# Kernel optimization log

Measured on AMD Instinct MI355X. Metric: run time of the kernel, lower is better.

The kernel has to match this reference:

```python
import jax, jax.numpy as jnp
import numpy as np

N = 100000   # nodes
E = 1000000  # edges
D = 64       # feature dim (all layers)
K = 3        # hops


def setup_inputs() -> dict:
    key = jax.random.key(0)
    ks = jax.random.split(key, 8)
    y = jax.random.normal(ks[0], (N, D), dtype=jnp.float32)
    edge_index = jax.random.randint(ks[1], (2, E), 0, N, dtype=jnp.int64)
    edge_weight = jax.random.uniform(ks[2], (E,), dtype=jnp.float32)
    # TAGConv layer l has K+1 linear maps (no bias) plus one output bias.
    s = 1.0 / np.sqrt(D)
    W1 = jax.random.uniform(ks[3], (K + 1, D, D), dtype=jnp.float32, minval=-s, maxval=s)
    b1 = jax.random.uniform(ks[4], (D,), dtype=jnp.float32, minval=-s, maxval=s)
    W2 = jax.random.uniform(ks[5], (K + 1, D, D), dtype=jnp.float32, minval=-s, maxval=s)
    b2 = jax.random.uniform(ks[6], (D,), dtype=jnp.float32, minval=-s, maxval=s)
    return {"y": y, "edge_index": edge_index, "edge_weight": edge_weight,
            "W1": W1, "b1": b1, "W2": W2, "b2": b2}


def _tagconv(x, src, dst, ew, W, b):
    # out = sum_{k=0..K} (A^k x) W_k + b, where (A x)[i] = sum_{e: dst=i} ew_e * x[src_e]
    out = x @ W[0]
    h = x
    for k in range(1, K + 1):
        h = jax.ops.segment_sum(ew[:, None] * h[src], dst, num_segments=N)
        out = out + h @ W[k]
    return out + b


def reference(y, edge_index, edge_weight, W1, b1, W2, b2):
    src, dst = edge_index[0], edge_index[1]
    # layer 1: TAGConv -> residual (Identity) -> leaky_relu (primal=True path)
    h = _tagconv(y, src, dst, edge_weight, W1, b1)
    y = jax.nn.leaky_relu(h + y)
    # layer 2
    h = _tagconv(y, src, dst, edge_weight, W2, b2)
    y = jax.nn.leaky_relu(h + y)
    return y
```

## Files before the change

### kernel.cpp

```cpp
#include <hip/hip_runtime.h>
#include <cstdint>
#include <cstddef>

#define DFEAT 64
#define LSLOPE 0.01f
#define BINSHIFT 9
#define BINCAP 6144
#define CHUNK 4096

typedef _Float16 h8 __attribute__((ext_vector_type(8)));
typedef _Float16 h4 __attribute__((ext_vector_type(4)));
typedef _Float16 h2 __attribute__((ext_vector_type(2)));
typedef float f4 __attribute__((ext_vector_type(4)));

__global__ void setup_kernel(const unsigned int* __restrict__ ei, int* flag,
                             int* __restrict__ binCnt) {
  __shared__ int cnt;
  if (threadIdx.x == 0) cnt = 0;
  binCnt[threadIdx.x] = 0;
  __syncthreads();
  int z = 0;
  for (int i = threadIdx.x; i < 1024; i += blockDim.x)
    z += (ei[2 * i + 1] == 0u) ? 1 : 0;
  atomicAdd(&cnt, z);
  __syncthreads();
  if (threadIdx.x == 0) *flag = (cnt == 1024) ? 1 : 0;
}

__global__ void cvtprep_kernel(const float* __restrict__ in, _Float16* __restrict__ out,
                               int n4, const float* __restrict__ W1,
                               const float* __restrict__ W2, _Float16* __restrict__ Wt) {
  int i = blockIdx.x * blockDim.x + threadIdx.x;
  if (i < n4) {
    float4 v = ((const float4*)in)[i];
    h4 o;
    o[0] = (_Float16)v.x; o[1] = (_Float16)v.y;
    o[2] = (_Float16)v.z; o[3] = (_Float16)v.w;
    ((h4*)out)[i] = o;
  } else {
    int t = i - n4;
    if (t < 2 * 64 * 264) {
      int layer = t / (64 * 264);
      int r = t % (64 * 264);
      int c = r / 264;
      int kg = r % 264;
      float v = 0.f;
      if (kg < 256) {
        const float* W = layer ? W2 : W1;
        int a = kg >> 6, k = kg & 63;
        v = W[a * 4096 + k * 64 + c];
      }
      Wt[t] = (_Float16)v;
    }
  }
}

__global__ __launch_bounds__(256) void binA_kernel(
    const void* __restrict__ ei, const float* __restrict__ ew, int E,
    const int* __restrict__ flag, int* __restrict__ binCnt,
    int2* __restrict__ bins, int nbins) {
  __shared__ int hist[256];
  __shared__ int pref[256];
  __shared__ int lofs[256];
  __shared__ int gbase[256];
  __shared__ int2 pairs[CHUNK];
  int tid = threadIdx.x;
  int base = blockIdx.x * CHUNK;
  int nedge = E - base; if (nedge > CHUNK) nedge = CHUNK;
  for (int i = tid; i < nbins; i += 256) hist[i] = 0;
  __syncthreads();
  const bool is64 = (*flag != 0);
  for (int j = tid; j < nedge; j += 256) {
    int e = base + j;
    int d = is64 ? (int)((const long long*)ei)[(size_t)E + e]
                 : ((const int*)ei)[(size_t)E + e];
    atomicAdd(&hist[d >> BINSHIFT], 1);
  }
  __syncthreads();
  if (tid == 0) {
    int run = 0;
    for (int b = 0; b < nbins; ++b) { pref[b] = run; lofs[b] = run; run += hist[b]; }
  }
  __syncthreads();
  for (int j = tid; j < nedge; j += 256) {
    int e = base + j;
    int s, d;
    if (is64) { const long long* p = (const long long*)ei; s = (int)p[e]; d = (int)p[(size_t)E + e]; }
    else      { const int* p = (const int*)ei; s = p[e]; d = p[(size_t)E + e]; }
    int wq = (int)(ew[e] * 32768.0f + 0.5f);
    wq = wq > 32767 ? 32767 : wq;
    unsigned P = ((unsigned)s << 15) | (unsigned)wq;
    int pos = atomicAdd(&lofs[d >> BINSHIFT], 1);
    pairs[pos] = make_int2((int)P, d);
  }
  __syncthreads();
  for (int b = tid; b < nbins; b += 256)
    gbase[b] = (hist[b] > 0) ? atomicAdd(&binCnt[b], hist[b]) : 0;
  __syncthreads();
  for (int i = tid; i < nedge; i += 256) {
    int2 pr = pairs[i];
    int b = pr.y >> BINSHIFT;
    int off = gbase[b] + (i - pref[b]);
    if (off < BINCAP) bins[(size_t)b * BINCAP + off] = pr;
  }
}

__global__ __launch_bounds__(256) void binB_kernel(
    const int2* __restrict__ bins, const int* __restrict__ binCnt,
    int* __restrict__ rowptr, unsigned* __restrict__ ep, int nbins, int N) {
  __shared__ int ssum[256];
  __shared__ int cnt[512];
  __shared__ int ofs[512];
  int b = blockIdx.x, tid = threadIdx.x;
  ssum[tid] = (tid < nbins) ? binCnt[tid] : 0;
  __syncthreads();
  for (int off = 1; off < 256; off <<= 1) {
    int val = ssum[tid];
    int add = (tid >= off) ? ssum[tid - off] : 0;
    __syncthreads();
    ssum[tid] = val + add;
    __syncthreads();
  }
  int gstart = (b == 0) ? 0 : ssum[b - 1];
  if (b == nbins - 1 && tid == 0) rowptr[N] = ssum[nbins - 1];
  int nb = binCnt[b]; if (nb > BINCAP) nb = BINCAP;
  int dstBase = b << BINSHIFT;
  const int2* mybin = bins + (size_t)b * BINCAP;
  for (int i = tid; i < 512; i += 256) cnt[i] = 0;
  __syncthreads();
  for (int i = tid; i < nb; i += 256)
    atomicAdd(&cnt[mybin[i].y & 511], 1);
  __syncthreads();
  if (tid == 0) {
    int run = gstart;
    for (int k = 0; k < 512; ++k) { ofs[k] = run; run += cnt[k]; }
  }
  __syncthreads();
  for (int k = tid; k < 512; k += 256) {
    int d = dstBase + k;
    if (d < N) rowptr[d] = ofs[k];
  }
  __syncthreads();
  for (int i = tid; i < nb; i += 256) {
    int2 pr = mybin[i];
    int pos = atomicAdd(&ofs[pr.y & 511], 1);
    ep[pos] = (unsigned)pr.x;
  }
}

__device__ __forceinline__ void edge_fma(unsigned p, const uint4& v, float qs,
                                         h2& acc0, h2& acc1, h2& acc2, h2& acc3) {
  _Float16 wh = (_Float16)((float)(p & 32767u) * qs);
  h2 wp = {wh, wh};
  union { uint32_t u; h2 h; } cx, cy, cz, cw;
  cx.u = v.x; cy.u = v.y; cz.u = v.z; cw.u = v.w;
  acc0 += wp * cx.h; acc1 += wp * cy.h;
  acc2 += wp * cz.h; acc3 += wp * cw.h;
}

__global__ __launch_bounds__(256) void spmm_kernel(
    const _Float16* __restrict__ x, const int* __restrict__ rowptr,
    const unsigned* __restrict__ ep, _Float16* __restrict__ hout, int N) {
  int node = blockIdx.x * 32 + (threadIdx.x >> 3);
  if (node >= N) return;
  int fo = threadIdx.x & 7;
  int beg = rowptr[node], end = rowptr[node + 1];
  const float qs = 1.0f / 32768.0f;
  const uint4* __restrict__ xu = (const uint4*)x;
  h2 acc0 = {0, 0}, acc1 = {0, 0}, acc2 = {0, 0}, acc3 = {0, 0};
  int n = end - beg;
  if (n >= 4) {
    unsigned pa = ep[beg], pb = ep[beg + 1], pc = ep[beg + 2], pd = ep[beg + 3];
    uint4 va = xu[(size_t)(pa >> 15) * 8 + fo];
    uint4 vb = xu[(size_t)(pb >> 15) * 8 + fo];
    uint4 vc = xu[(size_t)(pc >> 15) * 8 + fo];
    uint4 vd = xu[(size_t)(pd >> 15) * 8 + fo];
    int i = beg + 4;
    for (; i + 3 < end; i += 4) {
      edge_fma(pa, va, qs, acc0, acc1, acc2, acc3);
      pa = ep[i];     va = xu[(size_t)(pa >> 15) * 8 + fo];
      edge_fma(pb, vb, qs, acc0, acc1, acc2, acc3);
      pb = ep[i + 1]; vb = xu[(size_t)(pb >> 15) * 8 + fo];
      edge_fma(pc, vc, qs, acc0, acc1, acc2, acc3);
      pc = ep[i + 2]; vc = xu[(size_t)(pc >> 15) * 8 + fo];
      edge_fma(pd, vd, qs, acc0, acc1, acc2, acc3);
      pd = ep[i + 3]; vd = xu[(size_t)(pd >> 15) * 8 + fo];
    }
    edge_fma(pa, va, qs, acc0, acc1, acc2, acc3);
    edge_fma(pb, vb, qs, acc0, acc1, acc2, acc3);
    edge_fma(pc, vc, qs, acc0, acc1, acc2, acc3);
    edge_fma(pd, vd, qs, acc0, acc1, acc2, acc3);
    for (; i < end; ++i) {
      unsigned p = ep[i];
      uint4 v = xu[(size_t)(p >> 15) * 8 + fo];
      edge_fma(p, v, qs, acc0, acc1, acc2, acc3);
    }
  } else {
    for (int i = beg; i < end; ++i) {
      unsigned p = ep[i];
      uint4 v = xu[(size_t)(p >> 15) * 8 + fo];
      edge_fma(p, v, qs, acc0, acc1, acc2, acc3);
    }
  }
  union { uint4 u; h2 h[4]; } o;
  o.h[0] = acc0; o.h[1] = acc1; o.h[2] = acc2; o.h[3] = acc3;
  ((uint4*)hout)[(size_t)node * 8 + fo] = o.u;
}

template <int OUTF16>
__global__ __launch_bounds__(256) void combine_mfma_kernel(
    const _Float16* __restrict__ x0, const _Float16* __restrict__ h1,
    const _Float16* __restrict__ h2v, const _Float16* __restrict__ h3,
    const _Float16* __restrict__ Wt, const float* __restrict__ b,
    const _Float16* __restrict__ resid, void* __restrict__ outp, int N) {
  __shared__ __align__(16) _Float16 Wl[64 * 264];

  int tid = threadIdx.x;
  {
    const uint32_t* g = (const uint32_t*)Wt;
    uint32_t* l = (uint32_t*)Wl;
    for (int i = tid; i < 64 * 132; i += 256) l[i] = g[i];
  }
  __syncthreads();

  int w = tid >> 6, lane = tid & 63;
  int l16 = lane & 15, lq = lane >> 4;
  int r0 = blockIdx.x * 128 + w * 32;

  f4 acc[2][4];
  f4 zero = {0.f, 0.f, 0.f, 0.f};
  #pragma unroll
  for (int rt = 0; rt < 2; ++rt)
    #pragma unroll
    for (int ct = 0; ct < 4; ++ct) acc[rt][ct] = zero;

  const _Float16* hops[4] = {x0, h1, h2v, h3};

  #pragma unroll
  for (int s = 0; s < 8; ++s) {
    const _Float16* __restrict__ Xa = hops[s >> 1];
    int kk = ((s & 1) << 5) + (lq << 3);
    int ra = r0 + l16;
    int rb = ra + 16;
    ra = ra < N ? ra : N - 1;
    rb = rb < N ? rb : N - 1;
    h8 A0 = *(const h8*)(Xa + (size_t)ra * DFEAT + kk);
    h8 A1 = *(const h8*)(Xa + (size_t)rb * DFEAT + kk);
    #pragma unroll
    for (int ct = 0; ct < 4; ++ct) {
      h8 B = *(const h8*)(Wl + (l16 + 16 * ct) * 264 + (s << 5) + (lq << 3));
      acc[0][ct] = __builtin_amdgcn_mfma_f32_16x16x32_f16(A0, B, acc[0][ct], 0, 0, 0);
      acc[1][ct] = __builtin_amdgcn_mfma_f32_16x16x32_f16(A1, B, acc[1][ct], 0, 0, 0);
    }
  }

  #pragma unroll
  for (int rt = 0; rt < 2; ++rt) {
    #pragma unroll
    for (int ct = 0; ct < 4; ++ct) {
      int col = 16 * ct + l16;
      float bb = b[col];
      #pragma unroll
      for (int reg = 0; reg < 4; ++reg) {
        int row = r0 + rt * 16 + lq * 4 + reg;
        if (row < N) {
          float v = acc[rt][ct][reg] + bb + (float)resid[(size_t)row * DFEAT + col];
          v = v > 0.f ? v : LSLOPE * v;
          if (OUTF16) ((_Float16*)outp)[(size_t)row * DFEAT + col] = (_Float16)v;
          else        ((float*)outp)[(size_t)row * DFEAT + col] = v;
        }
      }
    }
  }
}

extern "C" void kernel_launch(void* const* d_in, const int* in_sizes, int n_in,
                              void* d_out, int out_size, void* d_ws, size_t ws_size,
                              hipStream_t stream) {
  const float* y  = (const float*)d_in[0];
  const void*  ei = d_in[1];
  const float* ew = (const float*)d_in[2];
  const float* W1 = (const float*)d_in[3];
  const float* b1 = (const float*)d_in[4];
  const float* W2 = (const float*)d_in[5];
  const float* b2 = (const float*)d_in[6];
  float* out = (float*)d_out;

  const int N = in_sizes[0] / DFEAT;
  const int E = in_sizes[2];
  const size_t ND = (size_t)N * DFEAT;
  const int nbins = (N + (1 << BINSHIFT) - 1) >> BINSHIFT;

  _Float16* xh = (_Float16*)d_ws;
  _Float16* h1 = xh + ND;
  _Float16* h2b = h1 + ND;
  _Float16* h3 = h2b + ND;
  _Float16* o1 = h3 + ND;
  _Float16* Wt = o1 + ND;
  int* rowptr   = (int*)(((uintptr_t)(Wt + 2 * 64 * 264) + 255) & ~(uintptr_t)255);
  int* binCnt   = rowptr + (N + 1);
  int* flag     = binCnt + 256;
  int2* bins    = (int2*)(((uintptr_t)(flag + 1) + 255) & ~(uintptr_t)255);
  unsigned* ep  = (unsigned*)(bins + (size_t)nbins * BINCAP);

  const int n4 = (int)(ND / 4);
  const int cp_total = n4 + 2 * 64 * 264;

  setup_kernel<<<1, 256, 0, stream>>>((const unsigned int*)ei, flag, binCnt);
  cvtprep_kernel<<<(cp_total + 255) / 256, 256, 0, stream>>>(y, xh, n4, W1, W2, Wt);
  binA_kernel<<<(E + CHUNK - 1) / CHUNK, 256, 0, stream>>>(ei, ew, E, flag, binCnt, bins, nbins);
  binB_kernel<<<nbins, 256, 0, stream>>>(bins, binCnt, rowptr, ep, nbins, N);

  const int spmm_grid = (N + 31) / 32;
  const int comb_grid = (N + 127) / 128;

  spmm_kernel<<<spmm_grid, 256, 0, stream>>>(xh, rowptr, ep, h1, N);
  spmm_kernel<<<spmm_grid, 256, 0, stream>>>(h1, rowptr, ep, h2b, N);
  spmm_kernel<<<spmm_grid, 256, 0, stream>>>(h2b, rowptr, ep, h3, N);
  combine_mfma_kernel<1><<<comb_grid, 256, 0, stream>>>(xh, h1, h2b, h3, Wt, b1, xh, o1, N);
  spmm_kernel<<<spmm_grid, 256, 0, stream>>>(o1, rowptr, ep, h1, N);
  spmm_kernel<<<spmm_grid, 256, 0, stream>>>(h1, rowptr, ep, h2b, N);
  spmm_kernel<<<spmm_grid, 256, 0, stream>>>(h2b, rowptr, ep, h3, N);
  combine_mfma_kernel<0><<<comb_grid, 256, 0, stream>>>(o1, h1, h2b, h3, Wt + 64 * 264, b2, o1, out, N);
}
```

Measured before the change: 227.4 us.

## Fuse third-hop SpMM into the MFMA combine kernel via shared memory

The third SpMM hop is now computed inside the combine kernel. Each block gathers its 128 rows of the hop-3 result into an LDS tile, then runs the MFMA projection over all four hops, reading the first three from global memory. This removes one kernel launch per layer and the write and re-read of the h3 buffer. In exchange the combine kernel uses 512 threads with more LDS, and each wave now covers 16 rows instead of 32, so the SpMM gather and the MFMA work are serialized within a block.

```diff
diff --git a/kernel.cpp b/kernel.cpp
--- a/kernel.cpp
+++ b/kernel.cpp
@@ -158,15 +158,10 @@
   acc2 += wp * cz.h; acc3 += wp * cw.h;
 }
 
-__global__ __launch_bounds__(256) void spmm_kernel(
-    const _Float16* __restrict__ x, const int* __restrict__ rowptr,
-    const unsigned* __restrict__ ep, _Float16* __restrict__ hout, int N) {
-  int node = blockIdx.x * 32 + (threadIdx.x >> 3);
-  if (node >= N) return;
-  int fo = threadIdx.x & 7;
-  int beg = rowptr[node], end = rowptr[node + 1];
+__device__ __forceinline__ uint4 spmm_node(const uint4* __restrict__ xu,
+                                           const unsigned* __restrict__ ep,
+                                           int beg, int end, int fo) {
   const float qs = 1.0f / 32768.0f;
-  const uint4* __restrict__ xu = (const uint4*)x;
   h2 acc0 = {0, 0}, acc1 = {0, 0}, acc2 = {0, 0}, acc3 = {0, 0};
   int n = end - beg;
   if (n >= 4) {
@@ -204,71 +199,94 @@
   }
   union { uint4 u; h2 h[4]; } o;
   o.h[0] = acc0; o.h[1] = acc1; o.h[2] = acc2; o.h[3] = acc3;
-  ((uint4*)hout)[(size_t)node * 8 + fo] = o.u;
+  return o.u;
+}
+
+__global__ __launch_bounds__(256) void spmm_kernel(
+    const _Float16* __restrict__ x, const int* __restrict__ rowptr,
+    const unsigned* __restrict__ ep, _Float16* __restrict__ hout, int N) {
+  int node = blockIdx.x * 32 + (threadIdx.x >> 3);
+  if (node >= N) return;
+  int fo = threadIdx.x & 7;
+  uint4 r = spmm_node((const uint4*)x, ep, rowptr[node], rowptr[node + 1], fo);
+  ((uint4*)hout)[(size_t)node * 8 + fo] = r;
 }
 
 template <int OUTF16>
-__global__ __launch_bounds__(256) void combine_mfma_kernel(
+__global__ __launch_bounds__(512) void spmm_combine_kernel(
+    const _Float16* __restrict__ xg,
     const _Float16* __restrict__ x0, const _Float16* __restrict__ h1,
-    const _Float16* __restrict__ h2v, const _Float16* __restrict__ h3,
+    const _Float16* __restrict__ h2v,
+    const int* __restrict__ rowptr, const unsigned* __restrict__ ep,
     const _Float16* __restrict__ Wt, const float* __restrict__ b,
     const _Float16* __restrict__ resid, void* __restrict__ outp, int N) {
   __shared__ __align__(16) _Float16 Wl[64 * 264];
+  __shared__ __align__(16) _Float16 H3[128 * 72];
 
   int tid = threadIdx.x;
   {
     const uint32_t* g = (const uint32_t*)Wt;
     uint32_t* l = (uint32_t*)Wl;
-    for (int i = tid; i < 64 * 132; i += 256) l[i] = g[i];
+    for (int i = tid; i < 64 * 132; i += 512) l[i] = g[i];
+  }
+  {
+    int gid = tid >> 3, fo = tid & 7;
+    long long nb0 = (long long)blockIdx.x * 128;
+    #pragma unroll
+    for (int rep = 0; rep < 2; ++rep) {
+      int lr = gid + rep * 64;
+      long long node = nb0 + lr;
+      uint4 r = {0, 0, 0, 0};
+      if (node < N)
+        r = spmm_node((const uint4*)xg, ep, rowptr[node], rowptr[node + 1], fo);
+      *(uint4*)(H3 + lr * 72 + fo * 8) = r;
+    }
   }
   __syncthreads();
 
   int w = tid >> 6, lane = tid & 63;
   int l16 = lane & 15, lq = lane >> 4;
-  int r0 = blockIdx.x * 128 + w * 32;
-
-  f4 acc[2][4];
+  long long r0 = (long long)blockIdx.x * 128 + w * 16;
+  int lr0 = w * 16;
+
+  f4 acc[4];
   f4 zero = {0.f, 0.f, 0.f, 0.f};
   #pragma unroll
-  for (int rt = 0; rt < 2; ++rt)
-    #pragma unroll
-    for (int ct = 0; ct < 4; ++ct) acc[rt][ct] = zero;
-
-  const _Float16* hops[4] = {x0, h1, h2v, h3};
+  for (int ct = 0; ct < 4; ++ct) acc[ct] = zero;
+
+  const _Float16* hops[3] = {x0, h1, h2v};
 
   #pragma unroll
   for (int s = 0; s < 8; ++s) {
-    const _Float16* __restrict__ Xa = hops[s >> 1];
     int kk = ((s & 1) << 5) + (lq << 3);
-    int ra = r0 + l16;
-    int rb = ra + 16;
-    ra = ra < N ? ra : N - 1;
-    rb = rb < N ? rb : N - 1;
-    h8 A0 = *(const h8*)(Xa + (size_t)ra * DFEAT + kk);
-    h8 A1 = *(const h8*)(Xa + (size_t)rb * DFEAT + kk);
+    h8 A;
+    if (s < 6) {
+      const _Float16* __restrict__ Xa = hops[s >> 1];
+      long long ra = r0 + l16;
+      ra = ra < N ? ra : N - 1;
+      A = *(const h8*)(Xa + ra * DFEAT + kk);
+    } else {
+      A = *(const h8*)(H3 + (lr0 + l16) * 72 + kk);
+    }
     #pragma unroll
     for (int ct = 0; ct < 4; ++ct) {
       h8 B = *(const h8*)(Wl + (l16 + 16 * ct) * 264 + (s << 5) + (lq << 3));
-      acc[0][ct] = __builtin_amdgcn_mfma_f32_16x16x32_f16(A0, B, acc[0][ct], 0, 0, 0);
-      acc[1][ct] = __builtin_amdgcn_mfma_f32_16x16x32_f16(A1, B, acc[1][ct], 0, 0, 0);
+      acc[ct] = __builtin_amdgcn_mfma_f32_16x16x32_f16(A, B, acc[ct], 0, 0, 0);
     }
   }
 
   #pragma unroll
-  for (int rt = 0; rt < 2; ++rt) {
+  for (int ct = 0; ct < 4; ++ct) {
+    int col = 16 * ct + l16;
+    float bb = b[col];
     #pragma unroll
-    for (int ct = 0; ct < 4; ++ct) {
-      int col = 16 * ct + l16;
-      float bb = b[col];
-      #pragma unroll
-      for (int reg = 0; reg < 4; ++reg) {
-        int row = r0 + rt * 16 + lq * 4 + reg;
-        if (row < N) {
-          float v = acc[rt][ct][reg] + bb + (float)resid[(size_t)row * DFEAT + col];
-          v = v > 0.f ? v : LSLOPE * v;
-          if (OUTF16) ((_Float16*)outp)[(size_t)row * DFEAT + col] = (_Float16)v;
-          else        ((float*)outp)[(size_t)row * DFEAT + col] = v;
-        }
+    for (int reg = 0; reg < 4; ++reg) {
+      long long row = r0 + lq * 4 + reg;
+      if (row < N) {
+        float v = acc[ct][reg] + bb + (float)resid[row * DFEAT + col];
+        v = v > 0.f ? v : LSLOPE * v;
+        if (OUTF16) ((_Float16*)outp)[row * DFEAT + col] = (_Float16)v;
+        else        ((float*)outp)[row * DFEAT + col] = v;
       }
     }
   }
@@ -294,8 +312,7 @@
   _Float16* xh = (_Float16*)d_ws;
   _Float16* h1 = xh + ND;
   _Float16* h2b = h1 + ND;
-  _Float16* h3 = h2b + ND;
-  _Float16* o1 = h3 + ND;
+  _Float16* o1 = h2b + ND;
   _Float16* Wt = o1 + ND;
   int* rowptr   = (int*)(((uintptr_t)(Wt + 2 * 64 * 264) + 255) & ~(uintptr_t)255);
   int* binCnt   = rowptr + (N + 1);
@@ -316,10 +333,10 @@
 
   spmm_kernel<<<spmm_grid, 256, 0, stream>>>(xh, rowptr, ep, h1, N);
   spmm_kernel<<<spmm_grid, 256, 0, stream>>>(h1, rowptr, ep, h2b, N);
-  spmm_kernel<<<spmm_grid, 256, 0, stream>>>(h2b, rowptr, ep, h3, N);
-  combine_mfma_kernel<1><<<comb_grid, 256, 0, stream>>>(xh, h1, h2b, h3, Wt, b1, xh, o1, N);
+  spmm_combine_kernel<1><<<comb_grid, 512, 0, stream>>>(
+      h2b, xh, h1, h2b, rowptr, ep, Wt, b1, xh, o1, N);
   spmm_kernel<<<spmm_grid, 256, 0, stream>>>(o1, rowptr, ep, h1, N);
   spmm_kernel<<<spmm_grid, 256, 0, stream>>>(h1, rowptr, ep, h2b, N);
-  spmm_kernel<<<spmm_grid, 256, 0, stream>>>(h2b, rowptr, ep, h3, N);
-  combine_mfma_kernel<0><<<comb_grid, 256, 0, stream>>>(o1, h1, h2b, h3, Wt + 64 * 264, b2, o1, out, N);
-}
+  spmm_combine_kernel<0><<<comb_grid, 512, 0, stream>>>(
+      h2b, o1, h1, h2b, rowptr, ep, Wt + 64 * 264, b2, o1, out, N);
+}
```

Result: slower. 232.8 us (+2.3%).

## Fuse SpMM and combine stages into one cooperative persistent kernel

Applied to the files above, without the earlier changes.

Replaces the eight separate SpMM/combine kernel launches with a single cooperative mega-kernel that runs every stage as a grid-stride phase, separated by grid-wide syncs. The goal is to remove per-launch overhead and the idle tail between dependent kernels. The cost is a grid capped at 1024 blocks, a combine phase that reloads the weights into LDS on each call, 36KB of LDS held even during the SpMM phases, and grid.sync barrier overhead. Fewer resident blocks may also reduce the latency hiding available to the gather-bound SpMM.

```diff
diff --git a/kernel.cpp b/kernel.cpp
--- a/kernel.cpp
+++ b/kernel.cpp
@@ -1,6 +1,9 @@
 #include <hip/hip_runtime.h>
+#include <hip/hip_cooperative_groups.h>
 #include <cstdint>
 #include <cstddef>
+
+namespace cg = cooperative_groups;
 
 #define DFEAT 64
 #define LSLOPE 0.01f
@@ -158,15 +161,10 @@
   acc2 += wp * cz.h; acc3 += wp * cw.h;
 }
 
-__global__ __launch_bounds__(256) void spmm_kernel(
-    const _Float16* __restrict__ x, const int* __restrict__ rowptr,
-    const unsigned* __restrict__ ep, _Float16* __restrict__ hout, int N) {
-  int node = blockIdx.x * 32 + (threadIdx.x >> 3);
-  if (node >= N) return;
-  int fo = threadIdx.x & 7;
-  int beg = rowptr[node], end = rowptr[node + 1];
+__device__ __forceinline__ uint4 spmm_node(const uint4* __restrict__ xu,
+                                           const unsigned* __restrict__ ep,
+                                           int beg, int end, int fo) {
   const float qs = 1.0f / 32768.0f;
-  const uint4* __restrict__ xu = (const uint4*)x;
   h2 acc0 = {0, 0}, acc1 = {0, 0}, acc2 = {0, 0}, acc3 = {0, 0};
   int n = end - beg;
   if (n >= 4) {
@@ -204,17 +202,32 @@
   }
   union { uint4 u; h2 h[4]; } o;
   o.h[0] = acc0; o.h[1] = acc1; o.h[2] = acc2; o.h[3] = acc3;
-  ((uint4*)hout)[(size_t)node * 8 + fo] = o.u;
+  return o.u;
+}
+
+__device__ __forceinline__ void spmm_phase(const _Float16* __restrict__ x,
+                                           const int* __restrict__ rowptr,
+                                           const unsigned* __restrict__ ep,
+                                           _Float16* __restrict__ hout, int N) {
+  int fo = threadIdx.x & 7;
+  int lid = threadIdx.x >> 3;
+  for (long long base = (long long)blockIdx.x * 32; base < N;
+       base += (long long)gridDim.x * 32) {
+    long long node = base + lid;
+    if (node < N) {
+      uint4 r = spmm_node((const uint4*)x, ep, rowptr[node], rowptr[node + 1], fo);
+      ((uint4*)hout)[node * 8 + fo] = r;
+    }
+  }
 }
 
 template <int OUTF16>
-__global__ __launch_bounds__(256) void combine_mfma_kernel(
+__device__ __forceinline__ void combine_phase(
+    _Float16* __restrict__ Wl,
     const _Float16* __restrict__ x0, const _Float16* __restrict__ h1,
     const _Float16* __restrict__ h2v, const _Float16* __restrict__ h3,
     const _Float16* __restrict__ Wt, const float* __restrict__ b,
     const _Float16* __restrict__ resid, void* __restrict__ outp, int N) {
-  __shared__ __align__(16) _Float16 Wl[64 * 264];
-
   int tid = threadIdx.x;
   {
     const uint32_t* g = (const uint32_t*)Wt;
@@ -225,53 +238,80 @@
 
   int w = tid >> 6, lane = tid & 63;
   int l16 = lane & 15, lq = lane >> 4;
-  int r0 = blockIdx.x * 128 + w * 32;
-
-  f4 acc[2][4];
-  f4 zero = {0.f, 0.f, 0.f, 0.f};
-  #pragma unroll
-  for (int rt = 0; rt < 2; ++rt)
+  const _Float16* hops[4] = {x0, h1, h2v, h3};
+
+  for (long long t0 = (long long)blockIdx.x * 128; t0 < N;
+       t0 += (long long)gridDim.x * 128) {
+    long long r0 = t0 + w * 32;
+
+    f4 acc[2][4];
+    f4 zero = {0.f, 0.f, 0.f, 0.f};
     #pragma unroll
-    for (int ct = 0; ct < 4; ++ct) acc[rt][ct] = zero;
-
-  const _Float16* hops[4] = {x0, h1, h2v, h3};
-
-  #pragma unroll
-  for (int s = 0; s < 8; ++s) {
-    const _Float16* __restrict__ Xa = hops[s >> 1];
-    int kk = ((s & 1) << 5) + (lq << 3);
-    int ra = r0 + l16;
-    int rb = ra + 16;
-    ra = ra < N ? ra : N - 1;
-    rb = rb < N ? rb : N - 1;
-    h8 A0 = *(const h8*)(Xa + (size_t)ra * DFEAT + kk);
-    h8 A1 = *(const h8*)(Xa + (size_t)rb * DFEAT + kk);
+    for (int rt = 0; rt < 2; ++rt)
+      #pragma unroll
+      for (int ct = 0; ct < 4; ++ct) acc[rt][ct] = zero;
+
     #pragma unroll
-    for (int ct = 0; ct < 4; ++ct) {
-      h8 B = *(const h8*)(Wl + (l16 + 16 * ct) * 264 + (s << 5) + (lq << 3));
-      acc[0][ct] = __builtin_amdgcn_mfma_f32_16x16x32_f16(A0, B, acc[0][ct], 0, 0, 0);
-      acc[1][ct] = __builtin_amdgcn_mfma_f32_16x16x32_f16(A1, B, acc[1][ct], 0, 0, 0);
-    }
-  }
-
-  #pragma unroll
-  for (int rt = 0; rt < 2; ++rt) {
+    for (int s = 0; s < 8; ++s) {
+      const _Float16* __restrict__ Xa = hops[s >> 1];
+      int kk = ((s & 1) << 5) + (lq << 3);
+      long long ra = r0 + l16;
+      long long rb = ra + 16;
+      ra = ra < N ? ra : N - 1;
+      rb = rb < N ? rb : N - 1;
+      h8 A0 = *(const h8*)(Xa + ra * DFEAT + kk);
+      h8 A1 = *(const h8*)(Xa + rb * DFEAT + kk);
+      #pragma unroll
+      for (int ct = 0; ct < 4; ++ct) {
+        h8 B = *(const h8*)(Wl + (l16 + 16 * ct) * 264 + (s << 5) + (lq << 3));
+        acc[0][ct] = __builtin_amdgcn_mfma_f32_16x16x32_f16(A0, B, acc[0][ct], 0, 0, 0);
+        acc[1][ct] = __builtin_amdgcn_mfma_f32_16x16x32_f16(A1, B, acc[1][ct], 0, 0, 0);
+      }
+    }
+
     #pragma unroll
-    for (int ct = 0; ct < 4; ++ct) {
-      int col = 16 * ct + l16;
-      float bb = b[col];
+    for (int rt = 0; rt < 2; ++rt) {
       #pragma unroll
-      for (int reg = 0; reg < 4; ++reg) {
-        int row = r0 + rt * 16 + lq * 4 + reg;
-        if (row < N) {
-          float v = acc[rt][ct][reg] + bb + (float)resid[(size_t)row * DFEAT + col];
-          v = v > 0.f ? v : LSLOPE * v;
-          if (OUTF16) ((_Float16*)outp)[(size_t)row * DFEAT + col] = (_Float16)v;
-          else        ((float*)outp)[(size_t)row * DFEAT + col] = v;
+      for (int ct = 0; ct < 4; ++ct) {
+        int col = 16 * ct + l16;
+        float bb = b[col];
+        #pragma unroll
+        for (int reg = 0; reg < 4; ++reg) {
+          long long row = r0 + rt * 16 + lq * 4 + reg;
+          if (row < N) {
+            float v = acc[rt][ct][reg] + bb + (float)resid[row * DFEAT + col];
+            v = v > 0.f ? v : LSLOPE * v;
+            if (OUTF16) ((_Float16*)outp)[row * DFEAT + col] = (_Float16)v;
+            else        ((float*)outp)[row * DFEAT + col] = v;
+          }
         }
       }
     }
   }
+}
+
+__global__ void __launch_bounds__(256, 4) mega_kernel(
+    const _Float16* xh, _Float16* h1, _Float16* h2b, _Float16* h3, _Float16* o1,
+    float* out, const _Float16* Wt, const float* b1, const float* b2,
+    const int* rowptr, const unsigned* ep, int N) {
+  cg::grid_group grid = cg::this_grid();
+  __shared__ __align__(16) _Float16 Wl[64 * 264];
+
+  spmm_phase(xh, rowptr, ep, h1, N);
+  grid.sync();
+  spmm_phase(h1, rowptr, ep, h2b, N);
+  grid.sync();
+  spmm_phase(h2b, rowptr, ep, h3, N);
+  grid.sync();
+  combine_phase<1>(Wl, xh, h1, h2b, h3, Wt, b1, xh, o1, N);
+  grid.sync();
+  spmm_phase(o1, rowptr, ep, h1, N);
+  grid.sync();
+  spmm_phase(h1, rowptr, ep, h2b, N);
+  grid.sync();
+  spmm_phase(h2b, rowptr, ep, h3, N);
+  grid.sync();
+  combine_phase<0>(Wl, o1, h1, h2b, h3, Wt + 64 * 264, b2, o1, out, N);
 }
 
 extern "C" void kernel_launch(void* const* d_in, const int* in_sizes, int n_in,
@@ -311,15 +351,16 @@
   binA_kernel<<<(E + CHUNK - 1) / CHUNK, 256, 0, stream>>>(ei, ew, E, flag, binCnt, bins, nbins);
   binB_kernel<<<nbins, 256, 0, stream>>>(bins, binCnt, rowptr, ep, nbins, N);
 
-  const int spmm_grid = (N + 31) / 32;
-  const int comb_grid = (N + 127) / 128;
-
-  spmm_kernel<<<spmm_grid, 256, 0, stream>>>(xh, rowptr, ep, h1, N);
-  spmm_kernel<<<spmm_grid, 256, 0, stream>>>(h1, rowptr, ep, h2b, N);
-  spmm_kernel<<<spmm_grid, 256, 0, stream>>>(h2b, rowptr, ep, h3, N);
-  combine_mfma_kernel<1><<<comb_grid, 256, 0, stream>>>(xh, h1, h2b, h3, Wt, b1, xh, o1, N);
-  spmm_kernel<<<spmm_grid, 256, 0, stream>>>(o1, rowptr, ep, h1, N);
-  spmm_kernel<<<spmm_grid, 256, 0, stream>>>(h1, rowptr, ep, h2b, N);
-  spmm_kernel<<<spmm_grid, 256, 0, stream>>>(h2b, rowptr, ep, h3, N);
-  combine_mfma_kernel<0><<<comb_grid, 256, 0, stream>>>(o1, h1, h2b, h3, Wt + 64 * 264, b2, o1, out, N);
-}
+  int maxb = 4;
+  hipOccupancyMaxActiveBlocksPerMultiprocessor(&maxb, (const void*)mega_kernel, 256, 0);
+  if (maxb < 1) maxb = 1;
+  long long mg = (long long)maxb * 256;
+  if (mg > 1024) mg = 1024;
+  int grid = (int)mg;
+
+  void* kargs[] = {(void*)&xh, (void*)&h1, (void*)&h2b, (void*)&h3, (void*)&o1,
+                   (void*)&out, (void*)&Wt, (void*)&b1, (void*)&b2,
+                   (void*)&rowptr, (void*)&ep, (void*)&N};
+  hipLaunchCooperativeKernel((const void*)mega_kernel, dim3(grid), dim3(256),
+                             kargs, 0, stream);
+}
```

Result: slower. 769.5 us (+238.3%).
